# Kernel optimization log

Measured on AMD Instinct MI355X. Metric: run time of the kernel, lower is better.

The kernel has to match this reference:

```python
import jax, jax.numpy as jnp
import numpy as np

N_NODES = 100000
N_EDGES = 1600000
D_IN = 128
D_HID = 128
D_OUT = 2
BN_EPS = 1e-5


def _sage_conv(x, src, dst, W_l, b_l, W_r):
    # PyG SAGEConv (aggr='mean'): out = lin_l(mean_{j in N(i)} x_j) + lin_r(x_i)
    # messages flow src -> dst
    agg = jax.ops.segment_sum(x[src], dst, num_segments=x.shape[0])
    deg = jax.ops.segment_sum(jnp.ones((src.shape[0],), x.dtype), dst,
                              num_segments=x.shape[0])
    mean = agg / jnp.maximum(deg, 1.0)[:, None]
    return mean @ W_l + b_l + x @ W_r


def _batch_norm(x, gamma, beta):
    # training-mode BatchNorm1d math over the node dimension (biased var)
    mu = jnp.mean(x, axis=0)
    var = jnp.var(x, axis=0)
    return (x - mu) * jax.lax.rsqrt(var + BN_EPS) * gamma + beta


def setup_inputs() -> dict:
    key = jax.random.key(0)
    ks = jax.random.split(key, 10)
    s = lambda d: 1.0 / np.sqrt(d)
    x = jax.random.normal(ks[0], (N_NODES, D_IN), dtype=jnp.float32)
    edge_index = jax.random.randint(ks[1], (2, N_EDGES), 0, N_NODES, dtype=jnp.int64)
    W1l = jax.random.uniform(ks[2], (D_IN, D_HID), jnp.float32, -s(D_IN), s(D_IN))
    b1 = jax.random.uniform(ks[3], (D_HID,), jnp.float32, -s(D_IN), s(D_IN))
    W1r = jax.random.uniform(ks[4], (D_IN, D_HID), jnp.float32, -s(D_IN), s(D_IN))
    W2l = jax.random.uniform(ks[5], (D_HID, D_OUT), jnp.float32, -s(D_HID), s(D_HID))
    b2 = jax.random.uniform(ks[6], (D_OUT,), jnp.float32, -s(D_HID), s(D_HID))
    W2r = jax.random.uniform(ks[7], (D_HID, D_OUT), jnp.float32, -s(D_HID), s(D_HID))
    gamma1 = jnp.ones((D_HID,), jnp.float32)
    beta1 = jnp.zeros((D_HID,), jnp.float32)
    gamma2 = jnp.ones((D_OUT,), jnp.float32)
    beta2 = jnp.zeros((D_OUT,), jnp.float32)
    return {"x": x, "edge_index": edge_index,
            "W1l": W1l, "b1": b1, "W1r": W1r, "gamma1": gamma1, "beta1": beta1,
            "W2l": W2l, "b2": b2, "W2r": W2r, "gamma2": gamma2, "beta2": beta2}


def reference(x, edge_index, W1l, b1, W1r, gamma1, beta1,
              W2l, b2, W2r, gamma2, beta2):
    src, dst = edge_index[0], edge_index[1]
    h = _sage_conv(x, src, dst, W1l, b1, W1r)
    h = _batch_norm(h, gamma1, beta1)
    h = jax.nn.relu(h)
    # dropout in eval mode = identity
    h = _sage_conv(h, src, dst, W2l, b2, W2r)
    h = _batch_norm(h, gamma2, beta2)
    return jax.nn.log_softmax(h, axis=1)
```

## Files before the change

### kernel.cpp

```cpp
#include <hip/hip_runtime.h>
#include <hip/hip_bf16.h>
#include <math.h>


#define DH 128
#define PAD 64
#define NPB 128
#define CAPB (NPB * PAD)
#define MAXBINS 1024
#define MAXCHUNK 6400
#define SENT 0xFFFFFFFFu

typedef short short8 __attribute__((ext_vector_type(8)));
typedef float float4v __attribute__((ext_vector_type(4)));
typedef float float2v __attribute__((ext_vector_type(2)));
typedef unsigned uint4v __attribute__((ext_vector_type(4)));

template <typename T> static __device__ __forceinline__ float tof(T v);
template <> __device__ __forceinline__ float tof<float>(float v) { return v; }
template <> __device__ __forceinline__ float tof<__hip_bfloat16>(__hip_bfloat16 v) {
  return __bfloat162float(v);
}

static __device__ __forceinline__ short f2bf_s(float f) {
  union { __hip_bfloat16 h; short s; } u;
  u.h = __float2bfloat16(f);
  return u.s;
}

static __device__ __forceinline__ float bf2f(short s) {
  union { unsigned u; float f; } c;
  c.u = ((unsigned)(unsigned short)s) << 16;
  return c.f;
}

static __device__ __forceinline__ float asf(unsigned u) {
  union { unsigned u; float f; } c;
  c.u = u;
  return c.f;
}

__global__ void k_probe(const unsigned* __restrict__ xw,
                        const unsigned* __restrict__ ew,
                        int* __restrict__ flags) {
  int t = threadIdx.x;
  unsigned wx = xw[(size_t)t * 23456 + 7];
  unsigned el = (wx >> 7) & 0xFFu;
  int sx = (el >= 0x60 && el <= 0x85) ? 1 : 0;
  unsigned we = ew[(size_t)t * 12000 + 1];
  int se = (we == 0) ? 1 : 0;
  __shared__ int c[2];
  if (t < 2) c[t] = 0;
  __syncthreads();
  atomicAdd(&c[0], sx);
  atomicAdd(&c[1], se);
  __syncthreads();
  if (t == 0) {
    flags[0] = (c[0] < 192) ? 1 : 0;
    flags[2] = (c[1] > 192) ? 1 : 0;
  }
}

template <typename FT>
static __device__ __forceinline__ void wt_one(const FT* __restrict__ W1l,
                                              const FT* __restrict__ W1r,
                                              short* __restrict__ WT, int idx) {
  int n = idx >> 8, k = idx & 255;
  float v = (k < 128) ? tof(W1l[k * 128 + n]) : tof(W1r[(k - 128) * 128 + n]);
  WT[n * 256 + k] = f2bf_s(v);
}
__global__ void k_xbwt(const void* __restrict__ x, const void* __restrict__ W1l,
                       const void* __restrict__ W1r, const int* __restrict__ flags,
                       __hip_bfloat162* __restrict__ xb, short* __restrict__ WT,
                       int total2) {
  int gi = blockIdx.x * blockDim.x + threadIdx.x;
  bool f32 = flags[0] != 0;
  if (gi < 32768) {
    if (f32) wt_one<float>((const float*)W1l, (const float*)W1r, WT, gi);
    else wt_one<__hip_bfloat16>((const __hip_bfloat16*)W1l, (const __hip_bfloat16*)W1r, WT, gi);
  }
  int i = gi - 32768;
  if (i >= 0 && i < total2) {
    if (f32) {
      float2 v = ((const float2*)x)[i];
      __hip_bfloat162 o;
      o.x = __float2bfloat16(v.x);
      o.y = __float2bfloat16(v.y);
      xb[i] = o;
    } else {
      xb[i] = ((const __hip_bfloat162*)x)[i];
    }
  }
}

template <typename IT>
static __device__ __forceinline__ void binscatter_agg_body(
    const IT* __restrict__ es, const IT* __restrict__ ed,
    int* __restrict__ binCnt, unsigned* __restrict__ pairs,
    int E, int N, int chunk, int NB) {
  __shared__ int cnt[MAXBINS];
  __shared__ int sc[MAXBINS];
  __shared__ int gbase[MAXBINS];
  __shared__ unsigned buf[MAXCHUNK];
  int t = threadIdx.x;
  int e0 = blockIdx.x * chunk;
  int e1 = min(e0 + chunk, E);
  int nE = e1 - e0;
  if (nE <= 0) return;

  for (int b = t; b < MAXBINS; b += 256) cnt[b] = 0;
  __syncthreads();
  for (int i = t; i < nE; i += 256) {
    int d = (int)ed[e0 + i];
    if ((unsigned)d >= (unsigned)N) d = 0;
    atomicAdd(&cnt[d >> 7], 1);
  }
  __syncthreads();
  for (int b = t; b < MAXBINS; b += 256) sc[b] = cnt[b];
  __syncthreads();
  for (int off = 1; off < MAXBINS; off <<= 1) {
    int v[MAXBINS / 256];
#pragma unroll
    for (int j = 0; j < MAXBINS / 256; ++j) {
      int b = t + j * 256;
      v[j] = (b >= off) ? sc[b - off] : 0;
    }
    __syncthreads();
#pragma unroll
    for (int j = 0; j < MAXBINS / 256; ++j) sc[t + j * 256] += v[j];
    __syncthreads();
  }
  for (int b = t; b < NB; b += 256) {
    int c = cnt[b];
    sc[b] -= c;
    int g = 0;
    if (c > 0) g = atomicAdd(&binCnt[b * 16], c);
    gbase[b] = g;
    cnt[b] = 0;
  }
  __syncthreads();
  for (int i = t; i < nE; i += 256) {
    int s = (int)es[e0 + i], d = (int)ed[e0 + i];
    if ((unsigned)s >= (unsigned)N) s = 0;
    if ((unsigned)d >= (unsigned)N) d = 0;
    int bin = d >> 7;
    int p = atomicAdd(&cnt[bin], 1);
    buf[sc[bin] + p] = ((unsigned)(d & (NPB - 1)) << 20) | (unsigned)s;
  }
  __syncthreads();
  for (int b = t; b < NB; b += 256) {
    int c = cnt[b];
    if (c == 0) continue;
    int g = gbase[b];
    if (g >= CAPB) continue;
    int cv = min(c, CAPB - g);
    unsigned* dst = pairs + (size_t)b * CAPB + g;
    const unsigned* srcp = buf + sc[b];
    for (int j = 0; j < cv; ++j) dst[j] = srcp[j];
  }
}
__launch_bounds__(256)
__global__ void k_binscatter_agg(const void* __restrict__ ev, const int* __restrict__ flags,
                                 int* __restrict__ binCnt, unsigned* __restrict__ pairs,
                                 int E, int N, int chunk, int NB) {
  if (flags[2]) binscatter_agg_body<long long>((const long long*)ev, (const long long*)ev + E,
                                               binCnt, pairs, E, N, chunk, NB);
  else          binscatter_agg_body<int>((const int*)ev, (const int*)ev + E,
                                         binCnt, pairs, E, N, chunk, NB);
}

__launch_bounds__(256)
__global__ void k_binbuild(const unsigned* __restrict__ pairs,
                           const int* __restrict__ binCnt,
                           int* __restrict__ deg_i, int* __restrict__ srcs_pad, int N) {
  __shared__ int cnt[NPB];
  __shared__ int lst[NPB * PAD];
  int bin = blockIdx.x;
  int t = threadIdx.x;
  for (int i = t; i < NPB; i += 256) cnt[i] = 0;
  for (int i = t; i < NPB * PAD; i += 256) lst[i] = 0;
  __syncthreads();
  int m = min(binCnt[bin * 16], CAPB);
  const unsigned* pp = pairs + (size_t)bin * CAPB;
  for (int i = t; i < m; i += 256) {
    unsigned u = pp[i];
    if (u == SENT) continue;
    int local = u >> 20;
    int s = u & 0xFFFFF;
    int r = atomicAdd(&cnt[local], 1);
    if (r < PAD) lst[local * PAD + r] = s;
  }
  __syncthreads();
  int base = bin * NPB;
  for (int i = t; i < NPB; i += 256) {
    int node = base + i;
    if (node < N) deg_i[node] = cnt[i];
  }
  for (int i = t; i < NPB * PAD; i += 256) {
    int node = base + (i >> 6);
    if (node < N) srcs_pad[(size_t)base * PAD + i] = lst[i];
  }
}

static __device__ __forceinline__ void accum8(float2v acc[4], uint4v u) {
#pragma unroll
  for (int i = 0; i < 4; ++i) {
    float2v p;
    p[0] = asf(u[i] << 16);
    p[1] = asf(u[i] & 0xFFFF0000u);
    acc[i] += p;
  }
}
static __device__ __forceinline__ uint4v maskv(uint4v v, int keep) {
  unsigned m = keep ? 0xFFFFFFFFu : 0u;
  uint4v r;
#pragma unroll
  for (int i = 0; i < 4; ++i) r[i] = v[i] & m;
  return r;
}
__launch_bounds__(256)
__global__ void k_gather(const unsigned* __restrict__ xbu,
                         const int* __restrict__ deg_i, const int* __restrict__ srcs_pad,
                         short* __restrict__ meanbs, int N) {
  int node = blockIdx.x * 4 + (threadIdx.x >> 6);
  int lane = threadIdx.x & 63;
  int g = lane >> 4, l = lane & 15;
  if (node >= N) return;
  int dg = deg_i[node];
  int cnt = min(dg, PAD);
  const int* sl = srcs_pad + (size_t)node * PAD;
  int srcv = sl[lane];
  const uint4v* xv = (const uint4v*)xbu;
  float2v acc[4];
#pragma unroll
  for (int i = 0; i < 4; ++i) acc[i] = (float2v){0.f, 0.f};

  if (cnt > 0) {
    int sA0 = __shfl(srcv, g);
    int sA1 = __shfl(srcv, 4 + g);
    int sA2 = __shfl(srcv, 8 + g);
    int sA3 = __shfl(srcv, 12 + g);
    uint4v a0 = xv[(size_t)sA0 * 16 + l];
    uint4v a1 = xv[(size_t)sA1 * 16 + l];
    uint4v a2 = xv[(size_t)sA2 * 16 + l];
    uint4v a3 = xv[(size_t)sA3 * 16 + l];
    uint4v b0, b1, b2, b3;
    bool hb = cnt > 16;
    if (hb) {
      int sB0 = __shfl(srcv, 16 + g);
      int sB1 = __shfl(srcv, 20 + g);
      int sB2 = __shfl(srcv, 24 + g);
      int sB3 = __shfl(srcv, 28 + g);
      b0 = xv[(size_t)sB0 * 16 + l];
      b1 = xv[(size_t)sB1 * 16 + l];
      b2 = xv[(size_t)sB2 * 16 + l];
      b3 = xv[(size_t)sB3 * 16 + l];
    }
    a0 = maskv(a0, g < cnt);
    a1 = maskv(a1, 4 + g < cnt);
    a2 = maskv(a2, 8 + g < cnt);
    a3 = maskv(a3, 12 + g < cnt);
    accum8(acc, a0);
    accum8(acc, a1);
    accum8(acc, a2);
    accum8(acc, a3);
    if (hb) {
      b0 = maskv(b0, 16 + g < cnt);
      b1 = maskv(b1, 20 + g < cnt);
      b2 = maskv(b2, 24 + g < cnt);
      b3 = maskv(b3, 28 + g < cnt);
      accum8(acc, b0);
      accum8(acc, b1);
      accum8(acc, b2);
      accum8(acc, b3);
    }
    for (int j = 32; j < cnt; j += 16) {
      int s0 = __shfl(srcv, j + g);
      int s1 = __shfl(srcv, j + 4 + g);
      int s2 = __shfl(srcv, j + 8 + g);
      int s3 = __shfl(srcv, j + 12 + g);
      uint4v v0 = xv[(size_t)s0 * 16 + l];
      uint4v v1 = xv[(size_t)s1 * 16 + l];
      uint4v v2 = xv[(size_t)s2 * 16 + l];
      uint4v v3 = xv[(size_t)s3 * 16 + l];
      v0 = maskv(v0, j + g < cnt);
      v1 = maskv(v1, j + 4 + g < cnt);
      v2 = maskv(v2, j + 8 + g < cnt);
      v3 = maskv(v3, j + 12 + g < cnt);
      accum8(acc, v0);
      accum8(acc, v1);
      accum8(acc, v2);
      accum8(acc, v3);
    }
  }

#pragma unroll
  for (int i = 0; i < 4; ++i) {
#pragma unroll
    for (int c = 0; c < 2; ++c) {
      acc[i][c] += __shfl_xor(acc[i][c], 16);
      acc[i][c] += __shfl_xor(acc[i][c], 32);
    }
  }
  if (g == 0) {
    float invd = 1.0f / fmaxf((float)dg, 1.0f);
    short8 o;
#pragma unroll
    for (int i = 0; i < 4; ++i) {
      o[2 * i]     = f2bf_s(acc[i][0] * invd);
      o[2 * i + 1] = f2bf_s(acc[i][1] * invd);
    }
    *(short8*)(meanbs + (size_t)node * DH + l * 8) = o;
  }
}

template <typename FT>
static __device__ __forceinline__ void layer1_body(
    const short* __restrict__ meanbs, const short* __restrict__ xbs,
    const short* __restrict__ WTs, const FT* __restrict__ b1,
    __hip_bfloat16* __restrict__ h1, float* __restrict__ st1,
    int N, int ntiles) {
  int w = threadIdx.x >> 6;
  int lane = threadIdx.x & 63;
  int m = lane & 15;
  int quad = lane >> 4;

  float bs[8], bq[8];
#pragma unroll
  for (int c = 0; c < 8; ++c) { bs[c] = 0.f; bq[c] = 0.f; }
  float bias[8];
#pragma unroll
  for (int c = 0; c < 8; ++c) bias[c] = tof(b1[c * 16 + m]);

  for (int tt = blockIdx.x; tt < ntiles; tt += gridDim.x) {
    int rowbase = tt * 64 + w * 16;
    int arowc = min(rowbase + m, N - 1);

    short8 afrag[8];
    const short* mr = meanbs + (size_t)arowc * DH;
#pragma unroll
    for (int kt = 0; kt < 4; ++kt)
      afrag[kt] = *(const short8*)(mr + kt * 32 + quad * 8);
    const short* xr = xbs + (size_t)arowc * DH;
#pragma unroll
    for (int kt = 0; kt < 4; ++kt)
      afrag[4 + kt] = *(const short8*)(xr + kt * 32 + quad * 8);

    float4v acc[8];
#pragma unroll
    for (int c = 0; c < 8; ++c) acc[c] = (float4v){0.f, 0.f, 0.f, 0.f};

#pragma unroll
    for (int kt = 0; kt < 8; ++kt) {
#pragma unroll
      for (int c = 0; c < 8; ++c) {
        short8 b = *(const short8*)(WTs + (c * 16 + m) * 256 + kt * 32 + quad * 8);
        acc[c] = __builtin_amdgcn_mfma_f32_16x16x32_bf16(afrag[kt], b, acc[c], 0, 0, 0);
      }
    }

#pragma unroll
    for (int c = 0; c < 8; ++c) {
      int col = c * 16 + m;
#pragma unroll
      for (int r = 0; r < 4; ++r) {
        int ro = rowbase + quad * 4 + r;
        float v = acc[c][r] + bias[c];
        if (ro < N) {
          h1[(size_t)ro * DH + col] = __float2bfloat16(v);
          bs[c] += v;
          bq[c] += v * v;
        }
      }
    }
  }

  __shared__ float lsum[4][128];
  __shared__ float lsq[4][128];
#pragma unroll
  for (int c = 0; c < 8; ++c) {
    float s = bs[c], q = bq[c];
    s += __shfl_xor(s, 16); s += __shfl_xor(s, 32);
    q += __shfl_xor(q, 16); q += __shfl_xor(q, 32);
    if (quad == 0) { lsum[w][c * 16 + m] = s; lsq[w][c * 16 + m] = q; }
  }
  __syncthreads();
  int t = threadIdx.x;
  if (t < 128) {
    float s = lsum[0][t] + lsum[1][t] + lsum[2][t] + lsum[3][t];
    float q = lsq[0][t] + lsq[1][t] + lsq[2][t] + lsq[3][t];
    unsafeAtomicAdd(&st1[t], s);
    unsafeAtomicAdd(&st1[128 + t], q);
  }
}
__launch_bounds__(256)
__global__ void k_layer1(const short* __restrict__ meanbs, const short* __restrict__ xbs,
                         const short* __restrict__ WTs, const void* __restrict__ b1,
                         const int* __restrict__ flags,
                         __hip_bfloat16* __restrict__ h1, float* __restrict__ st1,
                         int N, int ntiles) {
  if (flags[0])
    layer1_body<float>(meanbs, xbs, WTs, (const float*)b1, h1, st1, N, ntiles);
  else
    layer1_body<__hip_bfloat16>(meanbs, xbs, WTs, (const __hip_bfloat16*)b1,
                                h1, st1, N, ntiles);
}

template <typename FT>
static __device__ __forceinline__ void zr_body(
    const short* __restrict__ h1s, const float* __restrict__ stats1,
    const FT* __restrict__ g1, const FT* __restrict__ be1,
    const FT* __restrict__ W2l, const FT* __restrict__ W2r,
    float4* __restrict__ zr, int N) {
  __shared__ float sc[128], sh[128];
  int t = threadIdx.x;
  if (t < 128) {
    float invN = 1.0f / (float)N;
    float mu = stats1[t] * invN;
    float var = stats1[128 + t] * invN - mu * mu;
    float a = tof(g1[t]) * rsqrtf(var + 1e-5f);
    sc[t] = a;
    sh[t] = tof(be1[t]) - mu * a;
  }
  __syncthreads();
  int lane = t & 63, w = t >> 6;
  int g = lane >> 4, l = lane & 15;
  int f0 = l * 8;
  float scl[8], shl[8], wl0[8], wl1[8], wr0[8], wr1[8];
#pragma unroll
  for (int j = 0; j < 8; ++j) {
    int f = f0 + j;
    scl[j] = sc[f];
    shl[j] = sh[f];
    wl0[j] = tof(W2l[f * 2 + 0]);
    wl1[j] = tof(W2l[f * 2 + 1]);
    wr0[j] = tof(W2r[f * 2 + 0]);
    wr1[j] = tof(W2r[f * 2 + 1]);
  }
  int gw = blockIdx.x * 4 + w;
  int nw = gridDim.x * 4;
  for (int base = gw * 4; base < N; base += nw * 4) {
    int node = base + g;
    if (node < N) {
      short8 hv = *(const short8*)(h1s + (size_t)node * DH + f0);
      float z0 = 0.f, z1 = 0.f, r0 = 0.f, r1 = 0.f;
#pragma unroll
      for (int j = 0; j < 8; ++j) {
        float v = fmaxf(bf2f(hv[j]) * scl[j] + shl[j], 0.0f);
        z0 += v * wl0[j];
        z1 += v * wl1[j];
        r0 += v * wr0[j];
        r1 += v * wr1[j];
      }
#pragma unroll
      for (int off = 8; off >= 1; off >>= 1) {
        z0 += __shfl_xor(z0, off);
        z1 += __shfl_xor(z1, off);
        r0 += __shfl_xor(r0, off);
        r1 += __shfl_xor(r1, off);
      }
      if (l == 0) zr[node] = make_float4(z0, z1, r0, r1);
    }
  }
}
__launch_bounds__(256)
__global__ void k_zr(const __hip_bfloat16* __restrict__ h1, const float* __restrict__ st1,
                     const void* g1, const void* be1, const void* W2l, const void* W2r,
                     const int* __restrict__ flags, float4* __restrict__ zr, int N) {
  if (flags[0])
    zr_body<float>((const short*)h1, st1, (const float*)g1, (const float*)be1,
                   (const float*)W2l, (const float*)W2r, zr, N);
  else
    zr_body<__hip_bfloat16>((const short*)h1, st1, (const __hip_bfloat16*)g1,
                            (const __hip_bfloat16*)be1,
                            (const __hip_bfloat16*)W2l, (const __hip_bfloat16*)W2r, zr, N);
}

template <typename FT>
static __device__ __forceinline__ void h2_body(
    const float2* __restrict__ z2, const int* __restrict__ deg_i,
    const int* __restrict__ srcs_pad, const FT* __restrict__ b2,
    float2* __restrict__ h2, float* __restrict__ stats2, int N) {
  int lane = threadIdx.x & 63, w = threadIdx.x >> 6;
  int g = lane >> 4, l = lane & 15;
  float bs0 = 0.f, bs1 = 0.f, bq0 = 0.f, bq1 = 0.f;
  float bb0 = tof(b2[0]), bb1 = tof(b2[1]);
  int gw = blockIdx.x * 4 + w;
  int nw = gridDim.x * 4;
  for (int base = gw * 4; base < N; base += nw * 4) {
    int node = base + g;
    float za = 0.f, zb = 0.f;
    int dg_true = 0;
    if (node < N) {
      dg_true = deg_i[node];
      int cnt = min(dg_true, PAD);
      const int* sl = srcs_pad + (size_t)node * PAD;
      for (int j = l; j < cnt; j += 16) {
        float2 v = z2[2 * sl[j]];
        za += v.x;
        zb += v.y;
      }
    }
#pragma unroll
    for (int off = 8; off >= 1; off >>= 1) {
      za += __shfl_xor(za, off);
      zb += __shfl_xor(zb, off);
    }
    if (node < N && l == 0) {
      float dg = fmaxf((float)dg_true, 1.0f);
      float2 rw = z2[2 * node + 1];
      float h0 = za / dg + rw.x + bb0;
      float h1v = zb / dg + rw.y + bb1;
      h2[node] = make_float2(h0, h1v);
      bs0 += h0; bs1 += h1v; bq0 += h0 * h0; bq1 += h1v * h1v;
    }
  }
  bs0 += __shfl_xor(bs0, 16); bs0 += __shfl_xor(bs0, 32);
  bs1 += __shfl_xor(bs1, 16); bs1 += __shfl_xor(bs1, 32);
  bq0 += __shfl_xor(bq0, 16); bq0 += __shfl_xor(bq0, 32);
  bq1 += __shfl_xor(bq1, 16); bq1 += __shfl_xor(bq1, 32);
  __shared__ float red[4][4];
  if (lane == 0) { red[w][0] = bs0; red[w][1] = bs1; red[w][2] = bq0; red[w][3] = bq1; }
  __syncthreads();
  if (threadIdx.x < 4) {
    float a = red[0][threadIdx.x] + red[1][threadIdx.x] +
              red[2][threadIdx.x] + red[3][threadIdx.x];
    unsafeAtomicAdd(&stats2[threadIdx.x], a);
  }
}
__launch_bounds__(256)
__global__ void k_h2(const float4* __restrict__ zr, const int* __restrict__ deg_i,
                     const int* __restrict__ srcs_pad, const void* b2,
                     const int* __restrict__ flags,
                     float2* __restrict__ h2, float* __restrict__ stats2, int N) {
  if (flags[0])
    h2_body<float>((const float2*)zr, deg_i, srcs_pad, (const float*)b2, h2, stats2, N);
  else
    h2_body<__hip_bfloat16>((const float2*)zr, deg_i, srcs_pad,
                            (const __hip_bfloat16*)b2, h2, stats2, N);
}

template <typename FT>
static __device__ __forceinline__ void out_body(
    const float2* __restrict__ h2, const float* __restrict__ stats2,
    const FT* __restrict__ g2, const FT* __restrict__ be2,
    void* __restrict__ out, int N) {
  int i = blockIdx.x * blockDim.x + threadIdx.x;
  if (i >= N) return;
  float invN = 1.0f / (float)N;
  float mu0 = stats2[0] * invN, mu1 = stats2[1] * invN;
  float v0 = stats2[2] * invN - mu0 * mu0;
  float v1 = stats2[3] * invN - mu1 * mu1;
  float r0 = rsqrtf(v0 + 1e-5f), r1 = rsqrtf(v1 + 1e-5f);
  float2 h = h2[i];
  float y0 = (h.x - mu0) * r0 * tof(g2[0]) + tof(be2[0]);
  float y1 = (h.y - mu1) * r1 * tof(g2[1]) + tof(be2[1]);
  float mx = fmaxf(y0, y1);
  float lse = mx + logf(expf(y0 - mx) + expf(y1 - mx));
  float o0 = y0 - lse, o1 = y1 - lse;
  if (sizeof(FT) == 4) {
    ((float2*)out)[i] = make_float2(o0, o1);
  } else {
    __hip_bfloat162 o;
    o.x = __float2bfloat16(o0);
    o.y = __float2bfloat16(o1);
    ((__hip_bfloat162*)out)[i] = o;
  }
}
__global__ void k_out(const float2* __restrict__ h2, const float* __restrict__ stats2,
                      const void* g2, const void* be2, const int* __restrict__ flags,
                      void* __restrict__ out, int N) {
  if (flags[0]) out_body<float>(h2, stats2, (const float*)g2, (const float*)be2, out, N);
  else out_body<__hip_bfloat16>(h2, stats2, (const __hip_bfloat16*)g2,
                                (const __hip_bfloat16*)be2, out, N);
}

extern "C" void kernel_launch(void* const* d_in, const int* in_sizes, int n_in,
                              void* d_out, int out_size, void* d_ws, size_t ws_size,
                              hipStream_t stream) {
  int ix = 0, ie = 1, iW1l = 2, ib1 = 3, iW1r = 4, ig1 = 5, ibe1 = 6,
      iW2l = 7, ib2 = 8, iW2r = 9, ig2 = 10, ibe2 = 11;
  if (n_in == 12) {
    int best = -1, second = -1;
    for (int i = 0; i < 12; ++i) {
      if (best < 0 || in_sizes[i] > in_sizes[best]) { second = best; best = i; }
      else if (second < 0 || in_sizes[i] > in_sizes[second]) second = i;
    }
    ix = best; ie = second;
    int c16384 = 0, c128 = 0, c256 = 0, c2 = 0;
    for (int i = 0; i < 12; ++i) {
      if (i == ix || i == ie) continue;
      int s = in_sizes[i];
      if (s == 16384) { if (c16384++ == 0) iW1l = i; else iW1r = i; }
      else if (s == 128) { if (c128 == 0) ib1 = i; else if (c128 == 1) ig1 = i; else ibe1 = i; c128++; }
      else if (s == 256) { if (c256++ == 0) iW2l = i; else iW2r = i; }
      else { if (c2 == 0) ib2 = i; else if (c2 == 1) ig2 = i; else ibe2 = i; c2++; }
    }
  }

  const void* x   = d_in[ix];
  const void* ev  = d_in[ie];
  const void* W1l = d_in[iW1l];
  const void* b1  = d_in[ib1];
  const void* W1r = d_in[iW1r];
  const void* g1  = d_in[ig1];
  const void* be1 = d_in[ibe1];
  const void* W2l = d_in[iW2l];
  const void* b2  = d_in[ib2];
  const void* W2r = d_in[iW2r];
  const void* g2  = d_in[ig2];
  const void* be2 = d_in[ibe2];

  int N = in_sizes[ix] / DH;
  int E = in_sizes[ie] / 2;
  int nb = (N + 63) / 64;
  int NB = (N + NPB - 1) / NPB;

  int nblk = 1024;
  if ((E + nblk - 1) / nblk > MAXCHUNK) nblk = (E + MAXCHUNK - 1) / MAXCHUNK;
  int chunk = (E + nblk - 1) / nblk;

  char* ws = (char*)d_ws;
  size_t off = 0;
  auto alloc = [&](size_t b) { size_t o = off; off += (b + 255) & ~(size_t)255; return o; };
  size_t o_st1   = alloc(256 * 4);
  size_t o_st2   = alloc(4 * 4);
  size_t o_bcnt  = alloc((size_t)NB * 16 * 4);
  size_t zlen = off;
  size_t o_pairs = alloc((size_t)NB * CAPB * 4);
  size_t o_degi  = alloc((size_t)N * 4);
  size_t o_srcs  = alloc((size_t)N * PAD * 4);
  size_t o_xb    = alloc((size_t)N * DH * 2);
  size_t o_mean  = alloc((size_t)N * DH * 2);
  size_t o_h1    = alloc((size_t)N * DH * 2);
  size_t o_wt    = alloc(256 * 128 * 2);
  size_t o_zr    = alloc((size_t)N * 16);
  size_t o_h2    = alloc((size_t)N * 8);
  size_t o_flg   = alloc(64);

  float* st1  = (float*)(ws + o_st1);
  float* st2  = (float*)(ws + o_st2);
  int* bcnt   = (int*)(ws + o_bcnt);
  unsigned* pairs = (unsigned*)(ws + o_pairs);
  int* deg_i  = (int*)(ws + o_degi);
  int* srcs   = (int*)(ws + o_srcs);
  __hip_bfloat162* xb = (__hip_bfloat162*)(ws + o_xb);
  short* meanb = (short*)(ws + o_mean);
  __hip_bfloat16* h1 = (__hip_bfloat16*)(ws + o_h1);
  short* WT   = (short*)(ws + o_wt);
  float4* zrp = (float4*)(ws + o_zr);
  float2* h2p = (float2*)(ws + o_h2);
  int* flags  = (int*)(ws + o_flg);

  hipMemsetAsync(d_ws, 0, zlen, stream);

  int total2 = N * 64;
  k_probe<<<1, 256, 0, stream>>>((const unsigned*)x, (const unsigned*)ev, flags);
  k_xbwt<<<(total2 + 32768 + 255) / 256, 256, 0, stream>>>(x, W1l, W1r, flags, xb, WT, total2);
  k_binscatter_agg<<<nblk, 256, 0, stream>>>(ev, flags, bcnt, pairs, E, N, chunk, NB);
  k_binbuild<<<NB, 256, 0, stream>>>(pairs, bcnt, deg_i, srcs, N);
  k_gather<<<(N + 3) / 4, 256, 0, stream>>>((const unsigned*)xb, deg_i, srcs, meanb, N);
  k_layer1<<<nb, 256, 0, stream>>>(meanb, (const short*)xb, WT, b1,
                                   flags, h1, st1, N, nb);
  k_zr<<<2048, 256, 0, stream>>>(h1, st1, g1, be1, W2l, W2r, flags, zrp, N);
  k_h2<<<2048, 256, 0, stream>>>(zrp, deg_i, srcs, b2, flags, h2p, st2, N);
  k_out<<<(N + 255) / 256, 256, 0, stream>>>(h2p, st2, g2, be2, flags, d_out, N);
}
```

Baseline: 381.0 us.

## Stage layer-1 weights in swizzled LDS with persistent grid-stride blocks

The layer-1 MFMA kernel now copies the full 64KB bf16 weight matrix into shared memory once per block and reads B fragments from LDS instead of global/L2. The weight layout is XOR-swizzled at creation time to avoid LDS bank conflicts. The grid is capped at 512 blocks that loop over tiles so the copy is amortized, and the stats scratch reuses the weight LDS buffer. The 64KB LDS footprint limits occupancy and adds a per-block preload cost.

After: 334.7 us. 12.1% less time.

```diff
diff --git a/kernel.cpp b/kernel.cpp
--- a/kernel.cpp
+++ b/kernel.cpp
@@ -10,6 +10,7 @@
 #define MAXBINS 1024
 #define MAXCHUNK 6400
 #define SENT 0xFFFFFFFFu
+#define L1BLOCKS 512
 
 typedef short short8 __attribute__((ext_vector_type(8)));
 typedef float float4v __attribute__((ext_vector_type(4)));
@@ -67,7 +68,7 @@
                                               short* __restrict__ WT, int idx) {
   int n = idx >> 8, k = idx & 255;
   float v = (k < 128) ? tof(W1l[k * 128 + n]) : tof(W1r[(k - 128) * 128 + n]);
-  WT[n * 256 + k] = f2bf_s(v);
+  WT[n * 256 + (k ^ ((n & 7) << 3))] = f2bf_s(v);
 }
 __global__ void k_xbwt(const void* __restrict__ x, const void* __restrict__ W1l,
                        const void* __restrict__ W1r, const int* __restrict__ flags,
@@ -320,10 +321,21 @@
     const short* __restrict__ WTs, const FT* __restrict__ b1,
     __hip_bfloat16* __restrict__ h1, float* __restrict__ st1,
     int N, int ntiles) {
-  int w = threadIdx.x >> 6;
-  int lane = threadIdx.x & 63;
+  __shared__ short ldsWT[32768];
+  int t = threadIdx.x;
+  {
+    const uint4v* src = (const uint4v*)WTs;
+    uint4v* dst = (uint4v*)ldsWT;
+#pragma unroll
+    for (int i = 0; i < 16; ++i) dst[t + i * 256] = src[t + i * 256];
+  }
+  __syncthreads();
+
+  int w = t >> 6;
+  int lane = t & 63;
   int m = lane & 15;
   int quad = lane >> 4;
+  int xm = (m & 7) << 3;
 
   float bs[8], bq[8];
 #pragma unroll
@@ -352,9 +364,10 @@
 
 #pragma unroll
     for (int kt = 0; kt < 8; ++kt) {
+      int koff = (kt * 32 + quad * 8) ^ xm;
 #pragma unroll
       for (int c = 0; c < 8; ++c) {
-        short8 b = *(const short8*)(WTs + (c * 16 + m) * 256 + kt * 32 + quad * 8);
+        short8 b = *(const short8*)(ldsWT + (c * 16 + m) * 256 + koff);
         acc[c] = __builtin_amdgcn_mfma_f32_16x16x32_bf16(afrag[kt], b, acc[c], 0, 0, 0);
       }
     }
@@ -375,20 +388,20 @@
     }
   }
 
-  __shared__ float lsum[4][128];
-  __shared__ float lsq[4][128];
+  __syncthreads();
+  float* lsum = (float*)ldsWT;
+  float* lsq  = lsum + 512;
 #pragma unroll
   for (int c = 0; c < 8; ++c) {
     float s = bs[c], q = bq[c];
     s += __shfl_xor(s, 16); s += __shfl_xor(s, 32);
     q += __shfl_xor(q, 16); q += __shfl_xor(q, 32);
-    if (quad == 0) { lsum[w][c * 16 + m] = s; lsq[w][c * 16 + m] = q; }
-  }
-  __syncthreads();
-  int t = threadIdx.x;
+    if (quad == 0) { lsum[w * 128 + c * 16 + m] = s; lsq[w * 128 + c * 16 + m] = q; }
+  }
+  __syncthreads();
   if (t < 128) {
-    float s = lsum[0][t] + lsum[1][t] + lsum[2][t] + lsum[3][t];
-    float q = lsq[0][t] + lsq[1][t] + lsq[2][t] + lsq[3][t];
+    float s = lsum[0 * 128 + t] + lsum[1 * 128 + t] + lsum[2 * 128 + t] + lsum[3 * 128 + t];
+    float q = lsq[0 * 128 + t] + lsq[1 * 128 + t] + lsq[2 * 128 + t] + lsq[3 * 128 + t];
     unsafeAtomicAdd(&st1[t], s);
     unsafeAtomicAdd(&st1[128 + t], q);
   }
@@ -620,6 +633,8 @@
   if ((E + nblk - 1) / nblk > MAXCHUNK) nblk = (E + MAXCHUNK - 1) / MAXCHUNK;
   int chunk = (E + nblk - 1) / nblk;
 
+  int grid1 = (nb < L1BLOCKS) ? nb : L1BLOCKS;
+
   char* ws = (char*)d_ws;
   size_t off = 0;
   auto alloc = [&](size_t b) { size_t o = off; off += (b + 255) & ~(size_t)255; return o; };
@@ -660,8 +675,8 @@
   k_binscatter_agg<<<nblk, 256, 0, stream>>>(ev, flags, bcnt, pairs, E, N, chunk, NB);
   k_binbuild<<<NB, 256, 0, stream>>>(pairs, bcnt, deg_i, srcs, N);
   k_gather<<<(N + 3) / 4, 256, 0, stream>>>((const unsigned*)xb, deg_i, srcs, meanb, N);
-  k_layer1<<<nb, 256, 0, stream>>>(meanb, (const short*)xb, WT, b1,
-                                   flags, h1, st1, N, nb);
+  k_layer1<<<grid1, 256, 0, stream>>>(meanb, (const short*)xb, WT, b1,
+                                      flags, h1, st1, N, nb);
   k_zr<<<2048, 256, 0, stream>>>(h1, st1, g1, be1, W2l, W2r, flags, zrp, N);
   k_h2<<<2048, 256, 0, stream>>>(zrp, deg_i, srcs, b2, flags, h2p, st2, N);
   k_out<<<(N + 255) / 256, 256, 0, stream>>>(h2p, st2, g2, be2, flags, d_out, N);
```
